# Kernel optimization log

Hardware: AMD Instinct MI355X
Metric: run time of the kernel (lower is better)

The kernel has to match this reference:

```python
import math
import jax, jax.numpy as jnp
import numpy as np

B, C, N, T = 16, 64, 1024, 12


def setup_inputs() -> dict:
    key = jax.random.key(0)
    ks = jax.random.split(key, 12)
    s = 1.0 / math.sqrt(C)
    inp = {
        "input": jax.random.normal(ks[0], (B, C, N, T), dtype=jnp.float32),
        # 1x1 conv weights stored as [out_c, in_c] (squeeze of [C,C,1,1])
        "qw": jax.random.normal(ks[1], (C, C), dtype=jnp.float32) * s,
        "qb": jnp.zeros((C,), dtype=jnp.float32),
        "vw": jax.random.normal(ks[2], (C, C), dtype=jnp.float32) * s,
        "vb": jnp.zeros((C,), dtype=jnp.float32),
        "cw": jax.random.normal(ks[3], (C, C), dtype=jnp.float32) * s,
        "cb": jnp.zeros((C,), dtype=jnp.float32),
        # memory: xavier_uniform over (C, N)
        "memory": jax.random.uniform(ks[4], (C, N), dtype=jnp.float32,
                                      minval=-1.0, maxval=1.0) * math.sqrt(6.0 / (C + N)),
        # fc: Linear(2,8) -> ReLU -> Linear(8,1); torch Linear weight is [out,in]
        "fc1w": jax.random.normal(ks[5], (8, 2), dtype=jnp.float32) * (1.0 / math.sqrt(2.0)),
        "fc1b": jnp.zeros((8,), dtype=jnp.float32),
        "fc2w": jax.random.normal(ks[6], (1, 8), dtype=jnp.float32) * (1.0 / math.sqrt(8.0)),
        "fc2b": jnp.zeros((1,), dtype=jnp.float32),
    }
    return inp


def _conv1x1(x, w, b):
    # Conv2d(C,C,(1,1)) + ReLU (dropout is identity in eval)
    return jax.nn.relu(jnp.einsum('oc,bcnt->bont', w, x) + b[None, :, None, None])


def reference(input, qw, qb, vw, vb, cw, cb, memory, fc1w, fc1b, fc2w, fc2b):
    query = _conv1x1(input, qw, qb)           # [B,C,N,T]
    value = _conv1x1(input, vw, vb)           # [B,C,N,T]
    c = query.shape[1]
    inv_sqrt_c = 1.0 / math.sqrt(c)

    # dynamic adjacency 1: query x memory
    a1 = jax.nn.softmax(
        jax.nn.relu(jnp.einsum('bcnt,cm->bnm', query, memory) * inv_sqrt_c), axis=-1)
    # dynamic adjacency 2: time-pooled query self-similarity
    qs = query.sum(-1)                        # [B,C,N]
    a2 = jax.nn.softmax(
        jax.nn.relu(jnp.einsum('bcn,bcm->bnm', qs, qs) * inv_sqrt_c), axis=-1)

    adj_f = jnp.stack([a1, a2], axis=-1)      # [B,N,N,2]
    h = jax.nn.relu(adj_f @ fc1w.T + fc1b)    # [B,N,N,8]
    adj_f = jax.nn.softmax((h @ fc2w.T + fc2b)[..., 0], axis=-1)  # [B,N,N]

    # top-k mask (k = 0.8*N), scatter 1s at topk indices
    k = int(adj_f.shape[1] * 0.8)
    _, topk_idx = jax.lax.top_k(adj_f, k)     # [B,N,k]
    bsz, n, _ = adj_f.shape
    bi = jnp.arange(bsz)[:, None, None]
    ni = jnp.arange(n)[None, :, None]
    mask = jnp.zeros_like(adj_f).at[bi, ni, topk_idx].set(1.0)
    adj_f = adj_f * mask

    # aggregation: bmm over flattened (C*T)
    b_, cc, nn_, t = value.shape
    vr = value.transpose(0, 2, 1, 3).reshape(b_, nn_, cc * t)   # [B,N,C*T]
    agg = adj_f @ vr                                            # [B,N,C*T]
    agg = agg.reshape(b_, nn_, cc, t).transpose(0, 2, 1, 3)     # [B,C,N,T]

    return _conv1x1(agg, cw, cb)
```

## Files before the change

kernel.cpp:

```cpp
#include <hip/hip_runtime.h>

using u32 = unsigned int;
using u64 = unsigned long long;
using u16 = unsigned short;

typedef __attribute__((ext_vector_type(8))) short bf16x8;
typedef __attribute__((ext_vector_type(4))) float f32x4;

__device__ __forceinline__ u16 f2bf(float f) {
  u32 u = __float_as_uint(f);
  u += 0x7FFFu + ((u >> 16) & 1u);
  return (u16)(u >> 16);
}

__device__ __forceinline__ float wredMaxF(float v) {
#pragma unroll
  for (int o = 32; o > 0; o >>= 1) v = fmaxf(v, __shfl_xor(v, o, 64));
  return v;
}
__device__ __forceinline__ double wredSumD(double v) {
#pragma unroll
  for (int o = 32; o > 0; o >>= 1) v += __shfl_xor(v, o, 64);
  return v;
}
__device__ __forceinline__ void wsync() {
  __builtin_amdgcn_wave_barrier();
  __threadfence_block();
  __builtin_amdgcn_wave_barrier();
}

__global__ __launch_bounds__(256) void k_conv_qv(
    const float* __restrict__ x, const float* __restrict__ qw, const float* __restrict__ qb,
    const float* __restrict__ vw, const float* __restrict__ vb,
    double* __restrict__ qs64, float* __restrict__ qs32T, u16* __restrict__ vr)
{
  __shared__ float Xs[8 * 772];
  __shared__ float wqT[64 * 65];
  __shared__ float wvT[64 * 65];
  __shared__ float qbL[64], vbL[64];
  const int tid = threadIdx.x;
  const int b = blockIdx.y;
  const int n0 = blockIdx.x * 8;

#pragma unroll
  for (int j = 0; j < 16; ++j) {
    int idx = tid + 256 * j;
    int o = idx >> 6, c = idx & 63;
    wqT[c * 65 + o] = qw[idx];
    wvT[c * 65 + o] = vw[idx];
  }
  if (tid < 64) { qbL[tid] = qb[tid]; vbL[tid] = vb[tid]; }
#pragma unroll
  for (int j = 0; j < 6; ++j) {
    int q = tid + 256 * j;
    int pr = q / 3, s = q - pr * 3;
    int c = pr >> 3, nl = pr & 7;
    *(float4*)&Xs[nl * 772 + c * 12 + s * 4] =
        *(const float4*)&x[(((size_t)(b * 64 + c)) * 1024 + n0 + nl) * 12 + s * 4];
  }
  __syncthreads();

  const int co = tid & 63;
  const int nlA = tid >> 6;
  const int nlB = nlA + 4;
  double q0[12], q1[12];
  float v0[12], v1[12];
#pragma unroll
  for (int t = 0; t < 12; ++t) { q0[t] = 0.0; q1[t] = 0.0; v0[t] = 0.f; v1[t] = 0.f; }

  for (int c = 0; c < 64; ++c) {
    double wqv = (double)wqT[c * 65 + co];
    float wvv = wvT[c * 65 + co];
    float xA[12], xB[12];
    *(float4*)&xA[0] = *(float4*)&Xs[nlA * 772 + c * 12 + 0];
    *(float4*)&xA[4] = *(float4*)&Xs[nlA * 772 + c * 12 + 4];
    *(float4*)&xA[8] = *(float4*)&Xs[nlA * 772 + c * 12 + 8];
    *(float4*)&xB[0] = *(float4*)&Xs[nlB * 772 + c * 12 + 0];
    *(float4*)&xB[4] = *(float4*)&Xs[nlB * 772 + c * 12 + 4];
    *(float4*)&xB[8] = *(float4*)&Xs[nlB * 772 + c * 12 + 8];
#pragma unroll
    for (int t = 0; t < 12; ++t) {
      q0[t] = fma(wqv, (double)xA[t], q0[t]);
      q1[t] = fma(wqv, (double)xB[t], q1[t]);
      v0[t] += wvv * xA[t];
      v1[t] += wvv * xB[t];
    }
  }

  const float qbv = qbL[co];
  const float vbv = vbL[co];
  double sA = 0.0, sB = 0.0;
#pragma unroll
  for (int t = 0; t < 12; ++t) {
    float qa = fmaxf((float)q0[t] + qbv, 0.f);
    float qbf = fmaxf((float)q1[t] + qbv, 0.f);
    sA += (double)qa;
    sB += (double)qbf;
  }
  size_t ia = ((size_t)(b * 1024 + n0 + nlA)) * 64 + co;
  size_t ib = ((size_t)(b * 1024 + n0 + nlB)) * 64 + co;
  qs64[ia] = sA; qs64[ib] = sB;
  qs32T[((size_t)(b * 64 + co)) * 1024 + n0 + nlA] = (float)sA;
  qs32T[((size_t)(b * 64 + co)) * 1024 + n0 + nlB] = (float)sB;

  size_t vb0 = ((size_t)(b * 1024 + n0 + nlA)) * 768 + co * 12;
  size_t vb1 = ((size_t)(b * 1024 + n0 + nlB)) * 768 + co * 12;
#pragma unroll
  for (int i = 0; i < 6; ++i) {
    u32 p0 = (u32)f2bf(fmaxf(v0[2 * i] + vbv, 0.f)) | ((u32)f2bf(fmaxf(v0[2 * i + 1] + vbv, 0.f)) << 16);
    *(u32*)&vr[vb0 + 2 * i] = p0;
    u32 p1 = (u32)f2bf(fmaxf(v1[2 * i] + vbv, 0.f)) | ((u32)f2bf(fmaxf(v1[2 * i + 1] + vbv, 0.f)) << 16);
    *(u32*)&vr[vb1 + 2 * i] = p1;
  }
}

__global__ __launch_bounds__(256) void k_transpose_vr(const u16* __restrict__ vr, u16* __restrict__ vrT)
{
  __shared__ u16 Tt[64 * 72];
  const int tid = threadIdx.x;
  const int b = blockIdx.z;
  const int ct0 = blockIdx.x * 64;
  const int m0 = blockIdx.y * 64;
#pragma unroll
  for (int j = 0; j < 2; ++j) {
    int idx = tid + 256 * j;
    int r = idx >> 3, s = idx & 7;
    u16 tmp[8];
    *(uint4*)tmp = *(const uint4*)&vr[((size_t)(b * 1024 + m0 + r)) * 768 + ct0 + s * 8];
#pragma unroll
    for (int jj = 0; jj < 8; ++jj) Tt[(s * 8 + jj) * 72 + r] = tmp[jj];
  }
  __syncthreads();
#pragma unroll
  for (int j = 0; j < 2; ++j) {
    int idx = tid + 256 * j;
    int r2 = idx >> 3, s2 = idx & 7;
    *(uint4*)&vrT[((size_t)(b * 768 + ct0 + r2)) * 1024 + m0 + s2 * 8] =
        *(const uint4*)&Tt[r2 * 72 + s2 * 8];
  }
}

__global__ __launch_bounds__(256) void k_score(
    const double* __restrict__ qs64, const float* __restrict__ qs32T, const float* __restrict__ mem,
    float* __restrict__ S1, float* __restrict__ S2, int b0)
{
  __shared__ double As64[128 * 17];
  __shared__ float Bm[16 * 68];
  __shared__ float Bq[16 * 68];
  const int tid = threadIdx.x;
  const int g = blockIdx.z;
  const int b = b0 + g;
  const int m0 = blockIdx.x * 64;
  const int n0 = blockIdx.y * 128;

  const int mgi  = tid & 7;
  const int ngrp = tid >> 3;

  double acc1[4][8], acc2[4][8];
#pragma unroll
  for (int i = 0; i < 4; ++i)
#pragma unroll
    for (int k = 0; k < 8; ++k) { acc1[i][k] = 0.0; acc2[i][k] = 0.0; }

  for (int ph = 0; ph < 4; ++ph) {
    const int cb = ph * 16;
    __syncthreads();
#pragma unroll
    for (int j = 0; j < 8; ++j) {
      int idx = tid + 256 * j;
      int nl = idx >> 4, c = idx & 15;
      As64[nl * 17 + c] = qs64[((size_t)(b * 1024 + n0 + nl)) * 64 + cb + c];
    }
#pragma unroll
    for (int j = 0; j < 4; ++j) {
      int idx = tid + 256 * j;
      int c = idx >> 6, mm = idx & 63;
      Bm[c * 68 + mm] = mem[(size_t)(cb + c) * 1024 + m0 + mm];
      Bq[c * 68 + mm] = qs32T[((size_t)(b * 64 + cb + c)) * 1024 + m0 + mm];
    }
    __syncthreads();

    for (int c = 0; c < 16; ++c) {
      double a[4], af[4];
#pragma unroll
      for (int i = 0; i < 4; ++i) {
        a[i] = As64[(ngrp * 4 + i) * 17 + c];
        af[i] = (double)(float)a[i];
      }
      float bm8[8], bq8[8];
      *(float4*)&bm8[0] = *(float4*)&Bm[c * 68 + mgi * 8 + 0];
      *(float4*)&bm8[4] = *(float4*)&Bm[c * 68 + mgi * 8 + 4];
      *(float4*)&bq8[0] = *(float4*)&Bq[c * 68 + mgi * 8 + 0];
      *(float4*)&bq8[4] = *(float4*)&Bq[c * 68 + mgi * 8 + 4];
#pragma unroll
      for (int k = 0; k < 8; ++k) {
        double bmd = (double)bm8[k];
        double bqd = (double)bq8[k];
#pragma unroll
        for (int i = 0; i < 4; ++i) {
          acc1[i][k] = fma(a[i], bmd, acc1[i][k]);
          acc2[i][k] = fma(af[i], bqd, acc2[i][k]);
        }
      }
    }
  }
#pragma unroll
  for (int ni = 0; ni < 4; ++ni) {
    size_t off = ((size_t)g * 1024 + n0 + ngrp * 4 + ni) * 1024 + m0 + mgi * 8;
    float o1[8], o2[8];
#pragma unroll
    for (int k = 0; k < 8; ++k) {
      o1[k] = fmaxf((float)(0.125 * acc1[ni][k]), 0.f);
      o2[k] = fmaxf((float)(0.125 * acc2[ni][k]), 0.f);
    }
    *(float4*)&S1[off + 0] = *(float4*)&o1[0];
    *(float4*)&S1[off + 4] = *(float4*)&o1[4];
    *(float4*)&S2[off + 0] = *(float4*)&o2[0];
    *(float4*)&S2[off + 4] = *(float4*)&o2[4];
  }
}

__global__ __launch_bounds__(256) void k_row(
    const float* __restrict__ S1, const float* __restrict__ S2,
    const float* __restrict__ fc1w, const float* __restrict__ fc1b,
    const float* __restrict__ fc2w, const float* __restrict__ fc2b,
    u16* __restrict__ adj, int b0)
{
  __shared__ u32 histS[4][256];
  const int tid = threadIdx.x;
  const int wv = tid >> 6;
  const int lane = tid & 63;
  const int n = blockIdx.x * 4 + wv;
  const int g = blockIdx.y;

  float w10[8], w11[8], b1s[8], w2s[8];
#pragma unroll
  for (int h = 0; h < 8; ++h) {
    w10[h] = fc1w[2 * h];
    w11[h] = fc1w[2 * h + 1];
    b1s[h] = fc1b[h];
    w2s[h] = fc2w[h];
  }
  const float b2s = fc2b[0];

  const float* r1 = S1 + ((size_t)g * 1024 + n) * 1024;
  const float* r2 = S2 + ((size_t)g * 1024 + n) * 1024;
  const int e0 = lane * 16;
  float s1v[16], s2v[16];
#pragma unroll
  for (int k = 0; k < 4; ++k) {
    *(float4*)&s1v[4 * k] = *(const float4*)&r1[e0 + 4 * k];
    *(float4*)&s2v[4 * k] = *(const float4*)&r2[e0 + 4 * k];
  }

  float lm1 = s1v[0], lm2 = s2v[0];
#pragma unroll
  for (int j = 1; j < 16; ++j) { lm1 = fmaxf(lm1, s1v[j]); lm2 = fmaxf(lm2, s2v[j]); }
  const float m1 = wredMaxF(lm1);
  const float m2 = wredMaxF(lm2);

  float e1[16], e2[16];
  double ls1 = 0.0, ls2 = 0.0;
#pragma unroll
  for (int j = 0; j < 16; ++j) {
    e1[j] = (float)exp((double)(s1v[j] - m1));
    ls1 += (double)e1[j];
    e2[j] = (float)exp((double)(s2v[j] - m2));
    ls2 += (double)e2[j];
  }
  const float Z1f = (float)wredSumD(ls1);
  const float Z2f = (float)wredSumD(ls2);

  float zv[16];
#pragma unroll
  for (int j = 0; j < 16; ++j) {
    float a1 = e1[j] / Z1f;
    float a2 = e2[j] / Z2f;
    float acc = 0.f;
#pragma unroll
    for (int h = 0; h < 8; ++h) {
      float hp = __fmaf_rn(a2, w11[h], __fmaf_rn(a1, w10[h], 0.0f));
      hp = hp + b1s[h];
      float hr = fmaxf(hp, 0.f);
      acc = __fmaf_rn(hr, w2s[h], acc);
    }
    zv[j] = acc + b2s;
  }

  float lmz = zv[0];
#pragma unroll
  for (int j = 1; j < 16; ++j) lmz = fmaxf(lmz, zv[j]);
  const float mz = wredMaxF(lmz);
  float ez[16];
  double lsz = 0.0;
#pragma unroll
  for (int j = 0; j < 16; ++j) {
    ez[j] = (float)exp((double)(zv[j] - mz));
    lsz += (double)ez[j];
  }
  const float Zzf = (float)wredSumD(lsz);

  u32 kreg[16];
#pragma unroll
  for (int j = 0; j < 16; ++j) kreg[j] = __float_as_uint(ez[j] / Zzf);

  volatile u32* hp = &histS[wv][0];
  u32 target = 819u;
  u32 prefix = 0u;
  for (int pass = 0; pass < 4; ++pass) {
    const int sh = 24 - 8 * pass;
#pragma unroll
    for (int i = 0; i < 4; ++i) hp[4 * lane + i] = 0u;
    wsync();
    if (pass == 0) {
#pragma unroll
      for (int j = 0; j < 16; ++j) {
        u32 bin = kreg[j] >> 24;
        bool pending = true;
        while (true) {
          u64 rem = __ballot(pending);
          if (rem == 0ull) break;
          int ld = (int)__ffsll((long long)rem) - 1;
          u32 fb = __shfl(bin, ld, 64);
          bool mine = pending && (bin == fb);
          u64 grp = __ballot(mine);
          if (lane == ld) atomicAdd((u32*)&hp[fb], (u32)__popcll(grp));
          if (mine) pending = false;
        }
      }
    } else {
#pragma unroll
      for (int j = 0; j < 16; ++j) {
        u32 key = kreg[j];
        if ((key >> (sh + 8)) == prefix) atomicAdd((u32*)&hp[(key >> sh) & 255u], 1u);
      }
    }
    wsync();
    u32 h0 = hp[4 * lane + 0], h1 = hp[4 * lane + 1];
    u32 h2 = hp[4 * lane + 2], h3 = hp[4 * lane + 3];
    u32 part = h0 + h1 + h2 + h3;
    u32 sfx = part;
#pragma unroll
    for (int o = 1; o < 64; o <<= 1) {
      u32 vsh = __shfl_down(sfx, o, 64);
      if (lane + o < 64) sfx += vsh;
    }
    u32 after = sfx - part;
    u32 c3 = h3 + after;
    u32 c2 = h2 + c3;
    u32 c1 = h1 + c2;
    u32 c0 = h0 + c1;
    u32 mybyte = 0u, myabove = 0u;
    bool found = false;
    if (c0 >= target && c1 < target)    { mybyte = (u32)(4 * lane + 0); myabove = c1; found = true; }
    if (c1 >= target && c2 < target)    { mybyte = (u32)(4 * lane + 1); myabove = c2; found = true; }
    if (c2 >= target && c3 < target)    { mybyte = (u32)(4 * lane + 2); myabove = c3; found = true; }
    if (c3 >= target && after < target) { mybyte = (u32)(4 * lane + 3); myabove = after; found = true; }
    u64 fb = __ballot(found);
    int src = (int)__ffsll((long long)fb) - 1;
    u32 byte_ = (u32)__shfl((int)mybyte, src, 64);
    u32 above = (u32)__shfl((int)myabove, src, 64);
    prefix = (prefix << 8) | byte_;
    target -= above;
    wsync();
  }
  const u32 vkey = prefix;
  const u32 need_eq = target;

  int cnt = 0;
#pragma unroll
  for (int j = 0; j < 16; ++j) cnt += (kreg[j] == vkey) ? 1 : 0;
  u32 inc = (u32)cnt;
#pragma unroll
  for (int o = 1; o < 64; o <<= 1) {
    u32 nv = __shfl_up(inc, o, 64);
    if (lane >= o) inc += nv;
  }
  u32 run = inc - (u32)cnt;

  u16 ov[16];
#pragma unroll
  for (int j = 0; j < 16; ++j) {
    u32 kk = kreg[j];
    bool eq = (kk == vkey);
    bool keep = (kk > vkey) || (eq && (run < need_eq));
    if (eq) run += 1u;
    ov[j] = keep ? f2bf(__uint_as_float(kk)) : (u16)0;
  }
  u16* arow = adj + ((size_t)(b0 + g) * 1024 + n) * 1024 + e0;
  *(uint4*)&arow[0] = *(uint4*)&ov[0];
  *(uint4*)&arow[8] = *(uint4*)&ov[8];
}

__global__ __launch_bounds__(256) void k_gemm_agg(
    const u16* __restrict__ adj, const u16* __restrict__ vrT, float* __restrict__ agg)
{
  __shared__ u16 As[128 * 40];
  __shared__ u16 Bs[128 * 40];
  const int tid = threadIdx.x;
  const int b = blockIdx.z;
  const int n0 = blockIdx.y * 128;
  const int ct0 = blockIdx.x * 128;
  const int wid = tid >> 6;
  const int lane = tid & 63;
  const int l16 = lane & 15;
  const int quad = lane >> 4;
  const int wm = (wid >> 1) * 64;
  const int wn = (wid & 1) * 64;

  f32x4 acc[4][4];
#pragma unroll
  for (int i = 0; i < 4; ++i)
#pragma unroll
    for (int j = 0; j < 4; ++j) acc[i][j] = (f32x4)0.f;

  const u16* aG = adj + ((size_t)b * 1024 + n0) * 1024;
  const u16* bG = vrT + ((size_t)b * 768 + ct0) * 1024;

  for (int kt = 0; kt < 32; ++kt) {
    const int k0 = kt * 32;
    __syncthreads();
#pragma unroll
    for (int j = 0; j < 2; ++j) {
      int idx = tid + 256 * j;
      int row = idx >> 2, seg = idx & 3;
      *(uint4*)&As[row * 40 + seg * 8] = *(const uint4*)&aG[(size_t)row * 1024 + k0 + seg * 8];
      *(uint4*)&Bs[row * 40 + seg * 8] = *(const uint4*)&bG[(size_t)row * 1024 + k0 + seg * 8];
    }
    __syncthreads();
    bf16x8 af[4], bfv[4];
#pragma unroll
    for (int i = 0; i < 4; ++i) af[i] = *(bf16x8*)&As[(wm + i * 16 + l16) * 40 + quad * 8];
#pragma unroll
    for (int j = 0; j < 4; ++j) bfv[j] = *(bf16x8*)&Bs[(wn + j * 16 + l16) * 40 + quad * 8];
#pragma unroll
    for (int i = 0; i < 4; ++i)
#pragma unroll
      for (int j = 0; j < 4; ++j)
        acc[i][j] = __builtin_amdgcn_mfma_f32_16x16x32_bf16(af[i], bfv[j], acc[i][j], 0, 0, 0);
  }

#pragma unroll
  for (int i = 0; i < 4; ++i)
#pragma unroll
    for (int j = 0; j < 4; ++j)
#pragma unroll
      for (int r = 0; r < 4; ++r) {
        int row = n0 + wm + i * 16 + quad * 4 + r;
        int col = ct0 + wn + j * 16 + l16;
        agg[((size_t)b * 1024 + row) * 768 + col] = acc[i][j][r];
      }
}

__global__ __launch_bounds__(256) void k_convc(
    const float* __restrict__ agg, const float* __restrict__ cw,
    const float* __restrict__ cb, float* __restrict__ out)
{
  __shared__ float aggL[16 * 388];
  __shared__ float cwT[64 * 68];
  __shared__ float cbL[64];
  const int tid = threadIdx.x;
  const int b = blockIdx.y;
  const int n0 = blockIdx.x * 16;

#pragma unroll
  for (int j = 0; j < 16; ++j) {
    int idx = tid + 256 * j;
    int o = idx >> 6, c = idx & 63;
    cwT[c * 68 + o] = cw[idx];
  }
  if (tid < 64) cbL[tid] = cb[tid];

  const int o0 = (tid & 15) * 4;
  const int nl = tid >> 4;
  float acc[4][12];
#pragma unroll
  for (int oo = 0; oo < 4; ++oo)
#pragma unroll
    for (int t = 0; t < 12; ++t) acc[oo][t] = 0.f;

  for (int ph = 0; ph < 2; ++ph) {
    __syncthreads();
#pragma unroll
    for (int j = 0; j < 6; ++j) {
      int q4 = tid + 256 * j;
      int row = q4 / 96, wi = q4 - row * 96;
      *(float4*)&aggL[row * 388 + wi * 4] =
          *(const float4*)&agg[((size_t)(b * 1024 + n0 + row)) * 768 + ph * 384 + wi * 4];
    }
    __syncthreads();
    for (int cc = 0; cc < 32; ++cc) {
      int c = ph * 32 + cc;
      float4 w4 = *(float4*)&cwT[c * 68 + o0];
      float xr[12];
      *(float4*)&xr[0] = *(float4*)&aggL[nl * 388 + cc * 12 + 0];
      *(float4*)&xr[4] = *(float4*)&aggL[nl * 388 + cc * 12 + 4];
      *(float4*)&xr[8] = *(float4*)&aggL[nl * 388 + cc * 12 + 8];
#pragma unroll
      for (int t = 0; t < 12; ++t) {
        acc[0][t] += w4.x * xr[t];
        acc[1][t] += w4.y * xr[t];
        acc[2][t] += w4.z * xr[t];
        acc[3][t] += w4.w * xr[t];
      }
    }
  }

#pragma unroll
  for (int oo = 0; oo < 4; ++oo) {
    int o = o0 + oo;
    float bias = cbL[o];
    float ovv[12];
#pragma unroll
    for (int t = 0; t < 12; ++t) ovv[t] = fmaxf(acc[oo][t] + bias, 0.f);
    size_t base = ((size_t)(b * 64 + o) * 1024 + n0 + nl) * 12;
    *(float4*)&out[base + 0] = *(float4*)&ovv[0];
    *(float4*)&out[base + 4] = *(float4*)&ovv[4];
    *(float4*)&out[base + 8] = *(float4*)&ovv[8];
  }
}

extern "C" void kernel_launch(void* const* d_in, const int* in_sizes, int n_in,
                              void* d_out, int out_size, void* d_ws, size_t ws_size,
                              hipStream_t stream)
{
  const float* x    = (const float*)d_in[0];
  const float* qw   = (const float*)d_in[1];
  const float* qb   = (const float*)d_in[2];
  const float* vw   = (const float*)d_in[3];
  const float* vb   = (const float*)d_in[4];
  const float* cw   = (const float*)d_in[5];
  const float* cb   = (const float*)d_in[6];
  const float* mem  = (const float*)d_in[7];
  const float* fc1w = (const float*)d_in[8];
  const float* fc1b = (const float*)d_in[9];
  const float* fc2w = (const float*)d_in[10];
  const float* fc2b = (const float*)d_in[11];
  float* out = (float*)d_out;
  char* ws = (char*)d_ws;

  const size_t szQS64  = (size_t)16 * 1024 * 64 * 8;
  const size_t szQS32T = (size_t)16 * 1024 * 64 * 4;
  const size_t szVR    = (size_t)16 * 1024 * 768 * 2;
  const size_t szADJ   = (size_t)16 * 1024 * 1024 * 2;
  const size_t szAGG   = (size_t)16 * 1024 * 768 * 4;
  const size_t szSb    = (size_t)1024 * 1024 * 4;
  const size_t fixed   = szQS64 + szQS32T + 2 * szVR + szADJ + szAGG;

  int G = 16;
  while (G > 1 && (fixed + (size_t)2 * G * szSb) > ws_size) G >>= 1;

  double* qs64  = (double*)(ws);
  float*  qs32T = (float*)(ws + szQS64);
  u16*  vr      = (u16*)(ws + szQS64 + szQS32T);
  u16*  vrT     = (u16*)(ws + szQS64 + szQS32T + szVR);
  u16*  adj     = (u16*)(ws + szQS64 + szQS32T + 2 * szVR);
  float* agg    = (float*)(ws + szQS64 + szQS32T + 2 * szVR + szADJ);
  float* S1     = (float*)(ws + fixed);
  float* S2     = S1 + (size_t)G * 1024 * 1024;

  hipLaunchKernelGGL(k_conv_qv, dim3(128, 16), dim3(256), 0, stream, x, qw, qb, vw, vb, qs64, qs32T, vr);
  hipLaunchKernelGGL(k_transpose_vr, dim3(12, 16, 16), dim3(256), 0, stream, vr, vrT);
  for (int b0 = 0; b0 < 16; b0 += G) {
    hipLaunchKernelGGL(k_score, dim3(16, 8, G), dim3(256), 0, stream, qs64, qs32T, mem, S1, S2, b0);
    hipLaunchKernelGGL(k_row, dim3(256, G), dim3(256), 0, stream, S1, S2, fc1w, fc1b, fc2w, fc2b, adj, b0);
  }
  hipLaunchKernelGGL(k_gemm_agg, dim3(6, 8, 16), dim3(256), 0, stream, adj, vrT, agg);
  hipLaunchKernelGGL(k_convc, dim3(64, 16), dim3(256), 0, stream, agg, cw, cb, out);
}
```

Measured before the change: 573.1 us.

## Replace LDS radix-histogram top-k select with ballot bitwise search; inline fp64 exp

The per-row top-k threshold search no longer builds a shared-memory radix histogram with atomics over four passes. It now runs a 31-step bitwise binary search in which each step counts candidates with wave ballots and popcount, which removes LDS traffic, atomics and wave syncs at the cost of about 31×16 ballots per row. The library double-precision exp is also replaced with an inlined Cody-Waite reduction plus a Taylor polynomial, meant to avoid the generic exp's overhead while keeping near-fp64 accuracy.

```diff
diff --git a/kernel.cpp b/kernel.cpp
--- a/kernel.cpp
+++ b/kernel.cpp
@@ -23,10 +23,31 @@
   for (int o = 32; o > 0; o >>= 1) v += __shfl_xor(v, o, 64);
   return v;
 }
-__device__ __forceinline__ void wsync() {
-  __builtin_amdgcn_wave_barrier();
-  __threadfence_block();
-  __builtin_amdgcn_wave_barrier();
+
+__device__ __forceinline__ float fexpf64(double x) {
+  const double INVLN2 = 1.4426950408889634074;
+  const double NLN2HI = -6.93147180369123816490e-01;
+  const double NLN2LO = -1.90821492927058770002e-10;
+  double kd = rint(x * INVLN2);
+  double r = fma(kd, NLN2HI, x);
+  r = fma(kd, NLN2LO, r);
+  double p = 2.08767569878680990e-09;
+  p = fma(p, r, 2.50521083854417188e-08);
+  p = fma(p, r, 2.75573192239858907e-07);
+  p = fma(p, r, 2.75573192239858925e-06);
+  p = fma(p, r, 2.48015873015873016e-05);
+  p = fma(p, r, 1.98412698412698413e-04);
+  p = fma(p, r, 1.38888888888888889e-03);
+  p = fma(p, r, 8.33333333333333333e-03);
+  p = fma(p, r, 4.16666666666666667e-02);
+  p = fma(p, r, 1.66666666666666667e-01);
+  p = fma(p, r, 5.0e-01);
+  p = fma(p, r, 1.0);
+  p = fma(p, r, 1.0);
+  int k = (int)kd;
+  if (k < -1022) k = -1022;
+  double s = __hiloint2double((1023 + k) << 20, 0);
+  return (float)(p * s);
 }
 
 __global__ __launch_bounds__(256) void k_conv_qv(
@@ -226,7 +247,6 @@
     const float* __restrict__ fc2w, const float* __restrict__ fc2b,
     u16* __restrict__ adj, int b0)
 {
-  __shared__ u32 histS[4][256];
   const int tid = threadIdx.x;
   const int wv = tid >> 6;
   const int lane = tid & 63;
@@ -263,9 +283,9 @@
   double ls1 = 0.0, ls2 = 0.0;
 #pragma unroll
   for (int j = 0; j < 16; ++j) {
-    e1[j] = (float)exp((double)(s1v[j] - m1));
+    e1[j] = fexpf64((double)(s1v[j] - m1));
     ls1 += (double)e1[j];
-    e2[j] = (float)exp((double)(s2v[j] - m2));
+    e2[j] = fexpf64((double)(s2v[j] - m2));
     ls2 += (double)e2[j];
   }
   const float Z1f = (float)wredSumD(ls1);
@@ -295,7 +315,7 @@
   double lsz = 0.0;
 #pragma unroll
   for (int j = 0; j < 16; ++j) {
-    ez[j] = (float)exp((double)(zv[j] - mz));
+    ez[j] = fexpf64((double)(zv[j] - mz));
     lsz += (double)ez[j];
   }
   const float Zzf = (float)wredSumD(lsz);
@@ -304,68 +324,20 @@
 #pragma unroll
   for (int j = 0; j < 16; ++j) kreg[j] = __float_as_uint(ez[j] / Zzf);
 
-  volatile u32* hp = &histS[wv][0];
-  u32 target = 819u;
-  u32 prefix = 0u;
-  for (int pass = 0; pass < 4; ++pass) {
-    const int sh = 24 - 8 * pass;
-#pragma unroll
-    for (int i = 0; i < 4; ++i) hp[4 * lane + i] = 0u;
-    wsync();
-    if (pass == 0) {
-#pragma unroll
-      for (int j = 0; j < 16; ++j) {
-        u32 bin = kreg[j] >> 24;
-        bool pending = true;
-        while (true) {
-          u64 rem = __ballot(pending);
-          if (rem == 0ull) break;
-          int ld = (int)__ffsll((long long)rem) - 1;
-          u32 fb = __shfl(bin, ld, 64);
-          bool mine = pending && (bin == fb);
-          u64 grp = __ballot(mine);
-          if (lane == ld) atomicAdd((u32*)&hp[fb], (u32)__popcll(grp));
-          if (mine) pending = false;
-        }
-      }
-    } else {
-#pragma unroll
-      for (int j = 0; j < 16; ++j) {
-        u32 key = kreg[j];
-        if ((key >> (sh + 8)) == prefix) atomicAdd((u32*)&hp[(key >> sh) & 255u], 1u);
-      }
-    }
-    wsync();
-    u32 h0 = hp[4 * lane + 0], h1 = hp[4 * lane + 1];
-    u32 h2 = hp[4 * lane + 2], h3 = hp[4 * lane + 3];
-    u32 part = h0 + h1 + h2 + h3;
-    u32 sfx = part;
-#pragma unroll
-    for (int o = 1; o < 64; o <<= 1) {
-      u32 vsh = __shfl_down(sfx, o, 64);
-      if (lane + o < 64) sfx += vsh;
-    }
-    u32 after = sfx - part;
-    u32 c3 = h3 + after;
-    u32 c2 = h2 + c3;
-    u32 c1 = h1 + c2;
-    u32 c0 = h0 + c1;
-    u32 mybyte = 0u, myabove = 0u;
-    bool found = false;
-    if (c0 >= target && c1 < target)    { mybyte = (u32)(4 * lane + 0); myabove = c1; found = true; }
-    if (c1 >= target && c2 < target)    { mybyte = (u32)(4 * lane + 1); myabove = c2; found = true; }
-    if (c2 >= target && c3 < target)    { mybyte = (u32)(4 * lane + 2); myabove = c3; found = true; }
-    if (c3 >= target && after < target) { mybyte = (u32)(4 * lane + 3); myabove = after; found = true; }
-    u64 fb = __ballot(found);
-    int src = (int)__ffsll((long long)fb) - 1;
-    u32 byte_ = (u32)__shfl((int)mybyte, src, 64);
-    u32 above = (u32)__shfl((int)myabove, src, 64);
-    prefix = (prefix << 8) | byte_;
-    target -= above;
-    wsync();
-  }
-  const u32 vkey = prefix;
-  const u32 need_eq = target;
+  u32 vkey = 0u;
+  for (int bit = 30; bit >= 0; --bit) {
+    u32 cand = vkey | (1u << bit);
+    u32 cnt = 0u;
+#pragma unroll
+    for (int j = 0; j < 16; ++j)
+      cnt += (u32)__popcll(__ballot(kreg[j] >= cand));
+    if (cnt >= 819u) vkey = cand;
+  }
+  u32 cntGT = 0u;
+#pragma unroll
+  for (int j = 0; j < 16; ++j)
+    cntGT += (u32)__popcll(__ballot(kreg[j] > vkey));
+  const u32 need_eq = 819u - cntGT;
 
   int cnt = 0;
 #pragma unroll
```

New measurement: 512.1 us. 1.12x faster.
